# Performance work log

Measured on AMD Instinct MI355X. Metric: run time of the kernel, lower is better.

The kernel has to match this reference:

```python
import jax, jax.numpy as jnp
import numpy as np

D = 1024      # in_features
H = 8         # heads per branch (head_num // 2)
DH = (D // 2) // H  # 64
OUT = 1024

def _split_heads(x, B, S):
    # [B, S, D/2] -> [B, H, S, DH]
    return x.reshape(B, S, H, DH).transpose(0, 2, 1, 3)

def _attn(q, k, v):
    # q,k,v: [B, H, S, DH]
    scores = jnp.einsum('bhqd,bhkd->bhqk', q, k) / jnp.sqrt(jnp.float32(DH))
    a = jax.nn.softmax(scores, axis=-1)
    return jnp.einsum('bhqk,bhkd->bhqd', a, v)

def setup_inputs() -> dict:
    key = jax.random.key(0)
    ks = jax.random.split(key, 16)
    B, S = 2, 2048
    d2 = D // 2
    sc = lambda fan_in: 1.0 / np.sqrt(fan_in)
    inp = {
        'f1': jax.random.normal(ks[0], (B, S, D), jnp.float32),
        'f2': jax.random.normal(ks[1], (B, S, D), jnp.float32),
    }
    names = ['qs', 'ks', 'vs', 'qc', 'kc', 'vc']
    for i, n in enumerate(names):
        inp['W' + n] = jax.random.uniform(ks[2 + i], (d2, D), jnp.float32, -sc(D), sc(D))
        inp['b' + n] = jax.random.uniform(ks[8 + i], (d2,), jnp.float32, -sc(D), sc(D))
    inp['Wo'] = jax.random.uniform(ks[14], (OUT, 2 * D), jnp.float32, -sc(2 * D), sc(2 * D))
    inp['bo'] = jax.random.uniform(ks[15], (OUT,), jnp.float32, -sc(2 * D), sc(2 * D))
    return inp

def reference(f1, f2, Wqs, bqs, Wks, bks, Wvs, bvs, Wqc, bqc, Wkc, bkc, Wvc, bvc, Wo, bo):
    B, S, _ = f1.shape
    lin = lambda x, W, b: jax.nn.relu(x @ W.T + b)
    qs = lin(f1, Wqs, bqs); ks_ = lin(f1, Wks, bks); vs = lin(f1, Wvs, bvs)
    qc = lin(f1, Wqc, bqc); kc = lin(f2, Wkc, bkc); vc = lin(f2, Wvc, bvc)
    ys = _attn(_split_heads(qs, B, S), _split_heads(ks_, B, S), _split_heads(vs, B, S))
    yc = _attn(_split_heads(qc, B, S), _split_heads(kc, B, S), _split_heads(vc, B, S))
    merge = lambda y: y.transpose(0, 2, 1, 3).reshape(B, S, D // 2)
    # reshape_to_batches followed by reshape_from_batches on vs/vc is identity
    y = jnp.concatenate([merge(ys), merge(yc), vs, vc], axis=-1)  # [B, S, 2D]
    return jax.nn.relu(y @ Wo.T + bo)
```

## Files before the change

kernel.cpp:

```cpp
#include <hip/hip_runtime.h>
#include <hip/hip_bf16.h>

using bf16 = __hip_bfloat16;
typedef __attribute__((ext_vector_type(8))) short bf16x8;
typedef __attribute__((ext_vector_type(4))) float f32x4;
typedef __attribute__((ext_vector_type(16))) float f32x16;
typedef __attribute__((ext_vector_type(4))) unsigned int u32x4;

#define MTOT 4096

__device__ __forceinline__ f32x4 fzero() {
    f32x4 z = {0.f, 0.f, 0.f, 0.f};
    return z;
}
__device__ __forceinline__ f32x16 fzero16() {
    f32x16 z = {0.f,0.f,0.f,0.f,0.f,0.f,0.f,0.f,0.f,0.f,0.f,0.f,0.f,0.f,0.f,0.f};
    return z;
}

__device__ __forceinline__ f32x4 mfma16(bf16x8 a, bf16x8 b, f32x4 c) {
    return __builtin_amdgcn_mfma_f32_16x16x32_bf16(a, b, c, 0, 0, 0);
}
__device__ __forceinline__ f32x16 mfma32(bf16x8 a, bf16x8 b, f32x16 c) {
    return __builtin_amdgcn_mfma_f32_32x32x16_bf16(a, b, c, 0, 0, 0);
}

__device__ __forceinline__ float exp2_raw(float x) {
    float r;
    asm("v_exp_f32 %0, %1" : "=v"(r) : "v"(x));
    return r;
}

typedef const __attribute__((address_space(1))) unsigned int* gas_ptr;
typedef __attribute__((address_space(3))) unsigned int* las_ptr;
__device__ __forceinline__ void async_copy16(const bf16* g, bf16* l) {
    __builtin_amdgcn_global_load_lds((gas_ptr)(const void*)g, (las_ptr)(void*)l, 16, 0, 0);
}

__device__ __forceinline__ bf16x8 load8(const bf16* p) {
    return *(const bf16x8*)p;
}
__device__ __forceinline__ bf16x8 load8(const float* p) {
    float4 a = *(const float4*)p;
    float4 b = *(const float4*)(p + 4);
    bf16 t[8];
    t[0] = __float2bfloat16(a.x); t[1] = __float2bfloat16(a.y);
    t[2] = __float2bfloat16(a.z); t[3] = __float2bfloat16(a.w);
    t[4] = __float2bfloat16(b.x); t[5] = __float2bfloat16(b.y);
    t[6] = __float2bfloat16(b.z); t[7] = __float2bfloat16(b.w);
    return *(const bf16x8*)t;
}

__device__ __forceinline__ void store_out(bf16* C, size_t idx, float v) {
    C[idx] = __float2bfloat16(v);
}
__device__ __forceinline__ void store_out(float* C, size_t idx, float v) {
    C[idx] = v;
}

__global__ void MultiHeadSelfCrossAttention_7834020348638_kernel(float* out, int n) {
    int i = blockIdx.x * blockDim.x + threadIdx.x;
    if (i < n) out[i] = 0.25f;
}

struct CvtArgs {
    const float* src[9];
    bf16* dst[9];
    int n8[9];
};
__global__ void cvt_kernel(CvtArgs a) {
    int seg = blockIdx.y;
    int t = blockIdx.x * blockDim.x + threadIdx.x;
    if (t < a.n8[seg])
        *(bf16x8*)(a.dst[seg] + (size_t)t * 8) = load8(a.src[seg] + (size_t)t * 8);
}

template <int BN, typename TC>
__device__ __forceinline__ void gemm_fast(
    const bf16* __restrict__ A, int lda,
    const bf16* __restrict__ Bt, int ldb,
    const float* __restrict__ bias,
    TC* __restrict__ C, int ldc,
    int K, int m0, int n0)
{
    constexpr int NI  = BN / 32;
    constexpr int ACH = 128 * 64 / 8 / 256;
    constexpr int BCH = BN * 64 / 8 / 256;

    __shared__ bf16 As[128 * 64];
    __shared__ bf16 Bs[BN * 64];

    const int tid  = threadIdx.x;
    const int lane = tid & 63;
    const int l15  = lane & 15, quad = lane >> 4;
    const int wave = tid >> 6;
    const int wr   = wave >> 1, wc = wave & 1;

    f32x4 acc[4][NI];
#pragma unroll
    for (int mi = 0; mi < 4; mi++)
#pragma unroll
        for (int ni = 0; ni < NI; ni++)
            acc[mi][ni] = fzero();

    for (int k0 = 0; k0 < K; k0 += 64) {
        __syncthreads();
#pragma unroll
        for (int i = 0; i < ACH; i++) {
            int idx = i * 256 + tid;
            int r   = idx >> 3;
            int cg  = (idx & 7) * 8;
            async_copy16(A + (size_t)(m0 + r) * lda + k0 + cg, &As[idx * 8]);
        }
#pragma unroll
        for (int i = 0; i < BCH; i++) {
            int idx = i * 256 + tid;
            int r   = idx >> 3;
            int cg  = (idx & 7) * 8;
            async_copy16(Bt + (size_t)(n0 + r) * ldb + k0 + cg, &Bs[idx * 8]);
        }
        __syncthreads();

#pragma unroll
        for (int ks = 0; ks < 2; ks++) {
            bf16x8 af[4], bfr[NI];
#pragma unroll
            for (int mi = 0; mi < 4; mi++)
                af[mi] = *(const bf16x8*)&As[(wr * 64 + mi * 16 + l15) * 64 + ks * 32 + quad * 8];
#pragma unroll
            for (int ni = 0; ni < NI; ni++)
                bfr[ni] = *(const bf16x8*)&Bs[(wc * (BN / 2) + ni * 16 + l15) * 64 + ks * 32 + quad * 8];
#pragma unroll
            for (int mi = 0; mi < 4; mi++)
#pragma unroll
                for (int ni = 0; ni < NI; ni++)
                    acc[mi][ni] = mfma16(af[mi], bfr[ni], acc[mi][ni]);
        }
    }

#pragma unroll
    for (int ni = 0; ni < NI; ni++) {
        int col = n0 + wc * (BN / 2) + ni * 16 + l15;
        float bb = bias[col];
#pragma unroll
        for (int mi = 0; mi < 4; mi++) {
#pragma unroll
            for (int r = 0; r < 4; r++) {
                int row = m0 + wr * 64 + mi * 16 + quad * 4 + r;
                store_out(C, (size_t)row * ldc + col, fmaxf(acc[mi][ni][r] + bb, 0.f));
            }
        }
    }
}

template <int BN, typename TA, typename TB, typename TC>
__device__ __forceinline__ void gemm_reg(
    const TA* __restrict__ A, int lda,
    const TB* __restrict__ Bt, int ldb,
    const float* __restrict__ bias,
    TC* __restrict__ C, int ldc,
    int K, int m0, int n0)
{
    constexpr int NI  = BN / 32;
    constexpr int BCH = BN * 4 / 256;

    __shared__ bf16 As[128 * 32];
    __shared__ bf16 Bs[BN * 32];

    const int tid  = threadIdx.x;
    const int lane = tid & 63;
    const int l15  = lane & 15, quad = lane >> 4;
    const int wave = tid >> 6;
    const int wr   = wave >> 1, wc = wave & 1;

    f32x4 acc[4][NI];
#pragma unroll
    for (int mi = 0; mi < 4; mi++)
#pragma unroll
        for (int ni = 0; ni < NI; ni++)
            acc[mi][ni] = fzero();

    for (int k0 = 0; k0 < K; k0 += 32) {
        bf16x8 ra[2], rb[BCH];
#pragma unroll
        for (int i = 0; i < 2; i++) {
            int idx = i * 256 + tid;
            ra[i] = load8(A + (size_t)(m0 + (idx >> 2)) * lda + k0 + (idx & 3) * 8);
        }
#pragma unroll
        for (int i = 0; i < BCH; i++) {
            int idx = i * 256 + tid;
            rb[i] = load8(Bt + (size_t)(n0 + (idx >> 2)) * ldb + k0 + (idx & 3) * 8);
        }
        __syncthreads();
#pragma unroll
        for (int i = 0; i < 2; i++)
            *(bf16x8*)&As[(i * 256 + tid) * 8] = ra[i];
#pragma unroll
        for (int i = 0; i < BCH; i++)
            *(bf16x8*)&Bs[(i * 256 + tid) * 8] = rb[i];
        __syncthreads();

        bf16x8 af[4], bfr[NI];
#pragma unroll
        for (int mi = 0; mi < 4; mi++)
            af[mi] = *(const bf16x8*)&As[(wr * 64 + mi * 16 + l15) * 32 + quad * 8];
#pragma unroll
        for (int ni = 0; ni < NI; ni++)
            bfr[ni] = *(const bf16x8*)&Bs[(wc * (BN / 2) + ni * 16 + l15) * 32 + quad * 8];
#pragma unroll
        for (int mi = 0; mi < 4; mi++)
#pragma unroll
            for (int ni = 0; ni < NI; ni++)
                acc[mi][ni] = mfma16(af[mi], bfr[ni], acc[mi][ni]);
    }

#pragma unroll
    for (int ni = 0; ni < NI; ni++) {
        int col = n0 + wc * (BN / 2) + ni * 16 + l15;
        float bb = bias[col];
#pragma unroll
        for (int mi = 0; mi < 4; mi++) {
#pragma unroll
            for (int r = 0; r < 4; r++) {
                int row = m0 + wr * 64 + mi * 16 + quad * 4 + r;
                store_out(C, (size_t)row * ldc + col, fmaxf(acc[mi][ni][r] + bb, 0.f));
            }
        }
    }
}

__global__ void proj_fast(
    const bf16* __restrict__ F1, const bf16* __restrict__ F2,
    const bf16* __restrict__ Wb,
    const float* __restrict__ bqs, const float* __restrict__ bks,
    const float* __restrict__ bvs, const float* __restrict__ bqc,
    const float* __restrict__ bkc, const float* __restrict__ bvc,
    bf16* __restrict__ Y, bf16* Qs, bf16* Ks, bf16* Qc, bf16* Kc)
{
    const int g = blockIdx.z;
    const bf16* X; const float* bi; bf16* C; int ldc;
    switch (g) {
        case 0:  X = F1; bi = bqs; C = Qs;       ldc = 512;  break;
        case 1:  X = F1; bi = bks; C = Ks;       ldc = 512;  break;
        case 2:  X = F1; bi = bvs; C = Y + 1024; ldc = 2048; break;
        case 3:  X = F1; bi = bqc; C = Qc;       ldc = 512;  break;
        case 4:  X = F2; bi = bkc; C = Kc;       ldc = 512;  break;
        default: X = F2; bi = bvc; C = Y + 1536; ldc = 2048; break;
    }
    gemm_fast<128, bf16>(X, 1024, Wb + (size_t)g * 512 * 1024, 1024, bi, C, ldc,
                         1024, blockIdx.y * 128, blockIdx.x * 128);
}

__global__ void out_fast(const bf16* __restrict__ Y, const bf16* __restrict__ WoB,
                         const float* __restrict__ bo, float* __restrict__ out)
{
    gemm_fast<64, float>(Y, 2048, WoB, 2048, bo, out, 1024, 2048,
                         blockIdx.y * 128, blockIdx.x * 64);
}

__global__ void proj_reg(
    const float* __restrict__ f1, const float* __restrict__ f2,
    const float* __restrict__ Wqs, const float* __restrict__ bqs,
    const float* __restrict__ Wks, const float* __restrict__ bks,
    const float* __restrict__ Wvs, const float* __restrict__ bvs,
    const float* __restrict__ Wqc, const float* __restrict__ bqc,
    const float* __restrict__ Wkc, const float* __restrict__ bkc,
    const float* __restrict__ Wvc, const float* __restrict__ bvc,
    bf16* __restrict__ Y, bf16* Qs, bf16* Ks, bf16* Qc, bf16* Kc)
{
    const int g = blockIdx.z;
    const float *X, *W, *bi; bf16* C; int ldc;
    switch (g) {
        case 0:  X = f1; W = Wqs; bi = bqs; C = Qs;       ldc = 512;  break;
        case 1:  X = f1; W = Wks; bi = bks; C = Ks;       ldc = 512;  break;
        case 2:  X = f1; W = Wvs; bi = bvs; C = Y + 1024; ldc = 2048; break;
        case 3:  X = f1; W = Wqc; bi = bqc; C = Qc;       ldc = 512;  break;
        case 4:  X = f2; W = Wkc; bi = bkc; C = Kc;       ldc = 512;  break;
        default: X = f2; W = Wvc; bi = bvc; C = Y + 1536; ldc = 2048; break;
    }
    gemm_reg<128>(X, 1024, W, 1024, bi, C, ldc, 1024, blockIdx.y * 128, blockIdx.x * 128);
}

__global__ void out_reg(const bf16* __restrict__ Y, const float* __restrict__ Wo,
                        const float* __restrict__ bo, float* __restrict__ out)
{
    gemm_reg<64>(Y, 2048, Wo, 2048, bo, out, 1024, 2048, blockIdx.y * 128, blockIdx.x * 64);
}

__global__ void vt_kernel(const bf16* __restrict__ Y, bf16* __restrict__ VT) {
    const int tid = threadIdx.x;
    const int st = blockIdx.x, bh = blockIdx.y, br = blockIdx.z;
    const int b = bh >> 3, h = bh & 7;
    const bf16* src = Y + (size_t)b * 2048 * 2048 + 1024 + br * 512 + h * 64;
    bf16* dst = VT + ((size_t)((br * 2 + b) * 8 + h)) * 64 * 2048;
    const int s0 = st * 64;
#pragma unroll
    for (int i = 0; i < 2; i++) {
        int idx = i * 256 + tid;
        int d = idx >> 3, cs = (idx & 7) * 8;
        bf16 tmp[8];
#pragma unroll
        for (int j = 0; j < 8; j++)
            tmp[j] = src[(size_t)(s0 + cs + j) * 2048 + d];
        *(bf16x8*)&dst[(size_t)d * 2048 + s0 + cs] = *(const bf16x8*)tmp;
    }
}

__global__ __launch_bounds__(256, 4) void attn2_kernel(
    const bf16* __restrict__ Qsb, const bf16* __restrict__ Ksb,
    const bf16* __restrict__ Qcb, const bf16* __restrict__ Kcb,
    const bf16* __restrict__ VT, bf16* __restrict__ Y)
{
    __shared__ bf16 SMEM[4][64 * 64];

    const int tid  = threadIdx.x;
    const int lane = tid & 63;
    const int l31  = lane & 31;
    const int hi   = lane >> 5;
    const int wave = tid >> 6;

    const int lid   = blockIdx.x + 16 * blockIdx.y + 256 * blockIdx.z;
    const int xcd   = lid & 7, slot = lid >> 3;
    const int combo = xcd + 8 * (slot >> 4);
    const int qt    = slot & 15;
    const int bh    = combo & 15, br = combo >> 4;
    const int b = bh >> 3, h = bh & 7;

    const bf16* Qb = (br ? Qcb : Qsb) + (size_t)b * 2048 * 512 + h * 64;
    const bf16* Kb = (br ? Kcb : Ksb) + (size_t)b * 2048 * 512 + h * 64;
    const bf16* Vt = VT + ((size_t)((br * 2 + b) * 8 + h)) * 64 * 2048;
    bf16*       Ob = Y + (size_t)b * 2048 * 2048 + br * 512 + h * 64;
    const int q0 = qt * 128;

    bf16* QP = &SMEM[0][0];

#pragma unroll
    for (int i = 0; i < 4; i++) {
        int idx = i * 256 + tid;
        int r = idx >> 3, c0 = (idx & 7) * 8;
        *(bf16x8*)&QP[r * 72 + c0] = *(const bf16x8*)&Qb[(size_t)(q0 + r) * 512 + c0];
    }
    __syncthreads();

    bf16x8 qf[4];
#pragma unroll
    for (int kq = 0; kq < 4; kq++)
        qf[kq] = *(const bf16x8*)&QP[(wave * 32 + l31) * 72 + kq * 16 + hi * 8];
    __syncthreads();

#pragma unroll
    for (int i = 0; i < 2; i++) {
        int idx = i * 256 + tid;
        int r = idx >> 3, sl = (idx & 7) ^ (r & 7);
        async_copy16(Kb + (size_t)r * 512 + sl * 8, &SMEM[0][idx * 8]);
    }
#pragma unroll
    for (int i = 0; i < 2; i++) {
        int idx = i * 256 + tid;
        int r = idx >> 3, sl = (idx & 7) ^ (r & 7);
        async_copy16(Vt + (size_t)r * 2048 + sl * 8, &SMEM[1][idx * 8]);
    }
    __syncthreads();

    const short one_bits = (l31 == 0) ? (short)0x3F80 : (short)0;
    bf16x8 onesA;
#pragma unroll
    for (int j = 0; j < 8; j++) onesA[j] = one_bits;

    f32x16 o[2], ol;
    o[0] = fzero16(); o[1] = fzero16(); ol = fzero16();

    const float C1 = 0.18033688011112043f;
    const float C2 = -5.7707801635558535f;

    for (int jt = 0; jt < 32; jt++) {
        const int cur = jt & 1;
        const bf16* Kc = &SMEM[cur * 2][0];
        const bf16* Vc = &SMEM[cur * 2 + 1][0];

        if (jt < 31) {
            const size_t s0n = (size_t)(jt + 1) * 64;
            bf16* Kn = &SMEM[(cur ^ 1) * 2][0];
            bf16* Vn = &SMEM[(cur ^ 1) * 2 + 1][0];
#pragma unroll
            for (int i = 0; i < 2; i++) {
                int idx = i * 256 + tid;
                int r = idx >> 3, sl = (idx & 7) ^ (r & 7);
                async_copy16(Kb + (s0n + r) * 512 + sl * 8, &Kn[idx * 8]);
            }
#pragma unroll
            for (int i = 0; i < 2; i++) {
                int idx = i * 256 + tid;
                int r = idx >> 3, sl = (idx & 7) ^ (r & 7);
                async_copy16(Vt + (size_t)r * 2048 + s0n + sl * 8, &Vn[idx * 8]);
            }
        }

        f32x16 st[2];
        st[0] = fzero16(); st[1] = fzero16();
        __builtin_amdgcn_s_setprio(1);
#pragma unroll
        for (int t = 0; t < 2; t++)
#pragma unroll
            for (int kq = 0; kq < 4; kq++) {
                bf16x8 kf = *(const bf16x8*)&Kc[(t * 32 + l31) * 64
                               + (((kq * 2 + hi) ^ (l31 & 7)) * 8)];
                st[t] = mfma32(kf, qf[kq], st[t]);
            }
        __builtin_amdgcn_s_setprio(0);

        unsigned int pk[2][4][2];
#pragma unroll
        for (int t = 0; t < 2; t++)
#pragma unroll
            for (int g = 0; g < 4; g++) {
                float e0 = exp2_raw(fmaf(st[t][4 * g + 0], C1, C2));
                float e1 = exp2_raw(fmaf(st[t][4 * g + 1], C1, C2));
                float e2 = exp2_raw(fmaf(st[t][4 * g + 2], C1, C2));
                float e3 = exp2_raw(fmaf(st[t][4 * g + 3], C1, C2));
                asm("v_cvt_pk_bf16_f32 %0, %1, %2"
                    : "=v"(pk[t][g][0]) : "v"(e0), "v"(e1));
                asm("v_cvt_pk_bf16_f32 %0, %1, %2"
                    : "=v"(pk[t][g][1]) : "v"(e2), "v"(e3));
            }

        __builtin_amdgcn_s_setprio(1);
#pragma unroll
        for (int kb = 0; kb < 4; kb++) {
            const int t = kb >> 1, gb = (kb & 1) * 2;
            unsigned int u0 = pk[t][gb][0],     u1 = pk[t][gb][1];
            unsigned int v0 = pk[t][gb + 1][0], v1 = pk[t][gb + 1][1];
            asm("v_permlane32_swap_b32 %0, %1" : "+v"(u0), "+v"(v0));
            asm("v_permlane32_swap_b32 %0, %1" : "+v"(u1), "+v"(v1));
            u32x4 pw; pw.x = u0; pw.y = u1; pw.z = v0; pw.w = v1;
            bf16x8 pfrag = __builtin_bit_cast(bf16x8, pw);
#pragma unroll
            for (int dt = 0; dt < 2; dt++) {
                bf16x8 vf = *(const bf16x8*)&Vc[(dt * 32 + l31) * 64
                               + (((kb * 2 + hi) ^ (l31 & 7)) * 8)];
                o[dt] = mfma32(vf, pfrag, o[dt]);
            }
            ol = mfma32(onesA, pfrag, ol);
        }
        __builtin_amdgcn_s_setprio(0);

        __syncthreads();
    }

    const float linv = 1.0f / __shfl(ol[0], l31);
#pragma unroll
    for (int dt = 0; dt < 2; dt++)
#pragma unroll
        for (int r = 0; r < 16; r++) {
            int d = dt * 32 + (r & 3) + 8 * (r >> 2) + 4 * hi;
            QP[(wave * 32 + l31) * 72 + d] = __float2bfloat16(o[dt][r] * linv);
        }
    __syncthreads();
#pragma unroll
    for (int i = 0; i < 4; i++) {
        int idx = i * 256 + tid;
        int r = idx >> 3, c0 = (idx & 7) * 8;
        *(bf16x8*)&Ob[(size_t)(q0 + r) * 2048 + c0] = *(const bf16x8*)&QP[r * 72 + c0];
    }
}

__global__ __launch_bounds__(256, 4) void attn_kernel(
    const bf16* __restrict__ Qsb, const bf16* __restrict__ Ksb,
    const bf16* __restrict__ Qcb, const bf16* __restrict__ Kcb,
    bf16* __restrict__ Y)
{
    __shared__ bf16 QP[64 * 72];
    __shared__ bf16 Ksh[64 * 72];
    __shared__ bf16 Vsh[64 * 72];

    const int tid  = threadIdx.x;
    const int lane = tid & 63;
    const int l15  = lane & 15, quad = lane >> 4;
    const int wave = tid >> 6;
    const int qt = blockIdx.x, bh = blockIdx.y, br = blockIdx.z;
    const int b = bh >> 3, h = bh & 7;

    const bf16* Qb = (br ? Qcb : Qsb) + (size_t)b * 2048 * 512 + h * 64;
    const bf16* Kb = (br ? Kcb : Ksb) + (size_t)b * 2048 * 512 + h * 64;
    const bf16* Vb = Y + (size_t)b * 2048 * 2048 + 1024 + br * 512 + h * 64;
    bf16*       Ob = Y + (size_t)b * 2048 * 2048 +        br * 512 + h * 64;
    const int q0 = qt * 64;

#pragma unroll
    for (int i = 0; i < 2; i++) {
        int idx = i * 256 + tid;
        int r = idx >> 3, c0 = (idx & 7) * 8;
        *(bf16x8*)&QP[r * 72 + c0] = *(const bf16x8*)&Qb[(size_t)(q0 + r) * 512 + c0];
    }
    __syncthreads();

    bf16x8 qf[2];
#pragma unroll
    for (int ks = 0; ks < 2; ks++)
        qf[ks] = *(const bf16x8*)&QP[(wave * 16 + l15) * 72 + ks * 32 + quad * 8];

    const short one_bits = l15 == 0 ? (short)0x3F80 : (short)0;
    bf16x8 onesf;
#pragma unroll
    for (int j = 0; j < 8; j++) onesf[j] = one_bits;

    f32x4 o[4], o_l;
    o_l = fzero();
#pragma unroll
    for (int ni = 0; ni < 4; ni++) o[ni] = fzero();

    const int kr0 = tid >> 3, kc0 = (tid & 7) * 8;
    const int kr1 = (256 + tid) >> 3;

    bf16x8 kr[2], vr[2];
    kr[0] = *(const bf16x8*)&Kb[(size_t)kr0 * 512 + kc0];
    kr[1] = *(const bf16x8*)&Kb[(size_t)kr1 * 512 + kc0];
    vr[0] = *(const bf16x8*)&Vb[(size_t)lane * 2048 + (0 * 4 + wave) * 8];
    vr[1] = *(const bf16x8*)&Vb[(size_t)lane * 2048 + (1 * 4 + wave) * 8];

    for (int jt = 0; jt < 32; jt++) {
        __syncthreads();
        *(bf16x8*)&Ksh[kr0 * 72 + kc0] = kr[0];
        *(bf16x8*)&Ksh[kr1 * 72 + kc0] = kr[1];
#pragma unroll
        for (int i = 0; i < 2; i++) {
            int cg = i * 4 + wave;
            const bf16* e = (const bf16*)&vr[i];
#pragma unroll
            for (int j = 0; j < 8; j++)
                Vsh[(cg * 8 + j) * 72 + lane] = e[j];
        }
        __syncthreads();

        {
            const int s0n = (jt < 31) ? (jt + 1) * 64 : 31 * 64;
            kr[0] = *(const bf16x8*)&Kb[(size_t)(s0n + kr0) * 512 + kc0];
            kr[1] = *(const bf16x8*)&Kb[(size_t)(s0n + kr1) * 512 + kc0];
            vr[0] = *(const bf16x8*)&Vb[(size_t)(s0n + lane) * 2048 + (0 * 4 + wave) * 8];
            vr[1] = *(const bf16x8*)&Vb[(size_t)(s0n + lane) * 2048 + (1 * 4 + wave) * 8];
        }

        f32x4 s[4];
#pragma unroll
        for (int ni = 0; ni < 4; ni++) s[ni] = fzero();
#pragma unroll
        for (int ni = 0; ni < 4; ni++)
#pragma unroll
            for (int ks = 0; ks < 2; ks++) {
                bf16x8 kf = *(const bf16x8*)&Ksh[(ni * 16 + l15) * 72 + ks * 32 + quad * 8];
                s[ni] = mfma16(qf[ks], kf, s[ni]);
            }

#pragma unroll
        for (int ni = 0; ni < 4; ni++)
#pragma unroll
            for (int r = 0; r < 4; r++) {
                float p = __expf(s[ni][r] * 0.125f - 4.0f);
                QP[(wave * 16 + quad * 4 + r) * 72 + ni * 16 + l15] = __float2bfloat16(p);
            }

#pragma unroll
        for (int ks = 0; ks < 2; ks++) {
            bf16x8 pf = *(const bf16x8*)&QP[(wave * 16 + l15) * 72 + ks * 32 + quad * 8];
#pragma unroll
            for (int ni = 0; ni < 4; ni++) {
                bf16x8 vf = *(const bf16x8*)&Vsh[(ni * 16 + l15) * 72 + ks * 32 + quad * 8];
                o[ni] = mfma16(pf, vf, o[ni]);
            }
            o_l = mfma16(pf, onesf, o_l);
        }
    }

#pragma unroll
    for (int r = 0; r < 4; r++) {
        float lsum = __shfl(o_l[r], quad << 4);
        float inv = 1.f / lsum;
        int row = q0 + wave * 16 + quad * 4 + r;
#pragma unroll
        for (int ni = 0; ni < 4; ni++)
            Ob[(size_t)row * 2048 + ni * 16 + l15] = __float2bfloat16(o[ni][r] * inv);
    }
}

extern "C" void kernel_launch(void* const* d_in, const int* in_sizes, int n_in,
                              void* d_out, int out_size, void* d_ws, size_t ws_size,
                              hipStream_t stream) {
    const size_t out_bytes = (size_t)out_size * sizeof(float);
    const size_t ws_base = ((size_t)MTOT * 2048 + 4 * (size_t)MTOT * 512) * 2;
    const size_t ws_fast = ws_base + ((size_t)2 * MTOT * 1024 + 6 * 512 * 1024 + 1024 * 2048) * 2;
    const size_t vt_elems = (size_t)2 * 2 * 8 * 64 * 2048;
    const size_t ws_fast2 = ws_fast + vt_elems * 2;

    if (n_in != 16) { hipMemsetAsync(d_out, 0x43, out_bytes, stream); return; }
    if (ws_size < ws_base) { hipMemsetAsync(d_out, 0x41, out_bytes, stream); return; }

    const float* f1  = (const float*)d_in[0];
    const float* f2  = (const float*)d_in[1];
    const float* Wqs = (const float*)d_in[2];  const float* bqs = (const float*)d_in[3];
    const float* Wks = (const float*)d_in[4];  const float* bks = (const float*)d_in[5];
    const float* Wvs = (const float*)d_in[6];  const float* bvs = (const float*)d_in[7];
    const float* Wqc = (const float*)d_in[8];  const float* bqc = (const float*)d_in[9];
    const float* Wkc = (const float*)d_in[10]; const float* bkc = (const float*)d_in[11];
    const float* Wvc = (const float*)d_in[12]; const float* bvc = (const float*)d_in[13];
    const float* Wo  = (const float*)d_in[14]; const float* bo  = (const float*)d_in[15];

    bf16* Y  = (bf16*)d_ws;
    bf16* Qs = Y  + (size_t)MTOT * 2048;
    bf16* Ks = Qs + (size_t)MTOT * 512;
    bf16* Qc = Ks + (size_t)MTOT * 512;
    bf16* Kc = Qc + (size_t)MTOT * 512;
    float* out = (float*)d_out;

    if (ws_size >= ws_fast) {
        bf16* F1  = Kc + (size_t)MTOT * 512;
        bf16* F2  = F1 + (size_t)MTOT * 1024;
        bf16* Wb  = F2 + (size_t)MTOT * 1024;
        bf16* WoB = Wb + (size_t)6 * 512 * 1024;
        bf16* VT  = WoB + (size_t)1024 * 2048;

        CvtArgs ca;
        ca.src[0] = f1;  ca.dst[0] = F1;  ca.n8[0] = MTOT * 1024 / 8;
        ca.src[1] = f2;  ca.dst[1] = F2;  ca.n8[1] = MTOT * 1024 / 8;
        const float* ws_[6] = {Wqs, Wks, Wvs, Wqc, Wkc, Wvc};
        for (int i = 0; i < 6; i++) {
            ca.src[2 + i] = ws_[i];
            ca.dst[2 + i] = Wb + (size_t)i * 512 * 1024;
            ca.n8[2 + i]  = 512 * 1024 / 8;
        }
        ca.src[8] = Wo; ca.dst[8] = WoB; ca.n8[8] = 1024 * 2048 / 8;

        cvt_kernel<<<dim3((MTOT * 1024 / 8 + 255) / 256, 9), 256, 0, stream>>>(ca);
        proj_fast<<<dim3(4, 32, 6), 256, 0, stream>>>(
            F1, F2, Wb, bqs, bks, bvs, bqc, bkc, bvc, Y, Qs, Ks, Qc, Kc);
        if (ws_size >= ws_fast2) {
            vt_kernel<<<dim3(32, 16, 2), 256, 0, stream>>>(Y, VT);
            attn2_kernel<<<dim3(16, 16, 2), 256, 0, stream>>>(Qs, Ks, Qc, Kc, VT, Y);
        } else {
            attn_kernel<<<dim3(32, 16, 2), 256, 0, stream>>>(Qs, Ks, Qc, Kc, Y);
        }
        out_fast<<<dim3(16, 32), 256, 0, stream>>>(Y, WoB, bo, out);
    } else {
        proj_reg<<<dim3(4, 32, 6), 256, 0, stream>>>(
            f1, f2, Wqs, bqs, Wks, bks, Wvs, bvs, Wqc, bqc, Wkc, bkc, Wvc, bvc,
            Y, Qs, Ks, Qc, Kc);
        attn_kernel<<<dim3(32, 16, 2), 256, 0, stream>>>(Qs, Ks, Qc, Kc, Y);
        out_reg<<<dim3(16, 32), 256, 0, stream>>>(Y, Wo, bo, out);
    }
}
```

Measured before the change: 233.3 us.

## Fuse V transpose into projection epilogue and shrink GEMM tiles for occupancy

Removes the separate vt_kernel by having the projection GEMM epilogue write the transposed V (per head, d-major) directly into the VT buffer alongside the normal row-major output. The projection tile shrinks from 128x128 to 128x64 and the output GEMM tile from 128x64 to 64x64, with launch_bounds(256,4) on both, to launch more blocks and raise occupancy. This trades a kernel launch and an extra read of Y for scattered 8-byte transposed stores and smaller tiles with less data reuse per block.

```diff
diff --git a/kernel.cpp b/kernel.cpp
--- a/kernel.cpp
+++ b/kernel.cpp
@@ -3,6 +3,7 @@
 
 using bf16 = __hip_bfloat16;
 typedef __attribute__((ext_vector_type(8))) short bf16x8;
+typedef __attribute__((ext_vector_type(4))) short s16x4;
 typedef __attribute__((ext_vector_type(4))) float f32x4;
 typedef __attribute__((ext_vector_type(16))) float f32x16;
 typedef __attribute__((ext_vector_type(4))) unsigned int u32x4;
@@ -56,6 +57,9 @@
 }
 __device__ __forceinline__ void store_out(float* C, size_t idx, float v) {
     C[idx] = v;
+}
+__device__ __forceinline__ short bf16_bits(float v) {
+    return __builtin_bit_cast(short, __float2bfloat16(v));
 }
 
 __global__ void MultiHeadSelfCrossAttention_7834020348638_kernel(float* out, int n) {
@@ -75,19 +79,20 @@
         *(bf16x8*)(a.dst[seg] + (size_t)t * 8) = load8(a.src[seg] + (size_t)t * 8);
 }
 
-template <int BN, typename TC>
+template <int BM, int BN, typename TC>
 __device__ __forceinline__ void gemm_fast(
     const bf16* __restrict__ A, int lda,
     const bf16* __restrict__ Bt, int ldb,
     const float* __restrict__ bias,
     TC* __restrict__ C, int ldc,
-    int K, int m0, int n0)
-{
+    int K, int m0, int n0, bf16* __restrict__ VTW)
+{
+    constexpr int MI  = BM / 32;
     constexpr int NI  = BN / 32;
-    constexpr int ACH = 128 * 64 / 8 / 256;
+    constexpr int ACH = BM * 64 / 8 / 256;
     constexpr int BCH = BN * 64 / 8 / 256;
 
-    __shared__ bf16 As[128 * 64];
+    __shared__ bf16 As[BM * 64];
     __shared__ bf16 Bs[BN * 64];
 
     const int tid  = threadIdx.x;
@@ -96,9 +101,9 @@
     const int wave = tid >> 6;
     const int wr   = wave >> 1, wc = wave & 1;
 
-    f32x4 acc[4][NI];
-#pragma unroll
-    for (int mi = 0; mi < 4; mi++)
+    f32x4 acc[MI][NI];
+#pragma unroll
+    for (int mi = 0; mi < MI; mi++)
 #pragma unroll
         for (int ni = 0; ni < NI; ni++)
             acc[mi][ni] = fzero();
@@ -123,15 +128,15 @@
 
 #pragma unroll
         for (int ks = 0; ks < 2; ks++) {
-            bf16x8 af[4], bfr[NI];
-#pragma unroll
-            for (int mi = 0; mi < 4; mi++)
-                af[mi] = *(const bf16x8*)&As[(wr * 64 + mi * 16 + l15) * 64 + ks * 32 + quad * 8];
+            bf16x8 af[MI], bfr[NI];
+#pragma unroll
+            for (int mi = 0; mi < MI; mi++)
+                af[mi] = *(const bf16x8*)&As[(wr * (BM / 2) + mi * 16 + l15) * 64 + ks * 32 + quad * 8];
 #pragma unroll
             for (int ni = 0; ni < NI; ni++)
                 bfr[ni] = *(const bf16x8*)&Bs[(wc * (BN / 2) + ni * 16 + l15) * 64 + ks * 32 + quad * 8];
 #pragma unroll
-            for (int mi = 0; mi < 4; mi++)
+            for (int mi = 0; mi < MI; mi++)
 #pragma unroll
                 for (int ni = 0; ni < NI; ni++)
                     acc[mi][ni] = mfma16(af[mi], bfr[ni], acc[mi][ni]);
@@ -143,11 +148,21 @@
         int col = n0 + wc * (BN / 2) + ni * 16 + l15;
         float bb = bias[col];
 #pragma unroll
-        for (int mi = 0; mi < 4; mi++) {
-#pragma unroll
-            for (int r = 0; r < 4; r++) {
-                int row = m0 + wr * 64 + mi * 16 + quad * 4 + r;
-                store_out(C, (size_t)row * ldc + col, fmaxf(acc[mi][ni][r] + bb, 0.f));
+        for (int mi = 0; mi < MI; mi++) {
+            float v0 = fmaxf(acc[mi][ni][0] + bb, 0.f);
+            float v1 = fmaxf(acc[mi][ni][1] + bb, 0.f);
+            float v2 = fmaxf(acc[mi][ni][2] + bb, 0.f);
+            float v3 = fmaxf(acc[mi][ni][3] + bb, 0.f);
+            int row0 = m0 + wr * (BM / 2) + mi * 16 + quad * 4;
+            store_out(C, (size_t)(row0 + 0) * ldc + col, v0);
+            store_out(C, (size_t)(row0 + 1) * ldc + col, v1);
+            store_out(C, (size_t)(row0 + 2) * ldc + col, v2);
+            store_out(C, (size_t)(row0 + 3) * ldc + col, v3);
+            if (VTW) {
+                int d = wc * (BN / 2) + ni * 16 + l15;
+                int s = row0 & 2047;
+                short tv[4] = {bf16_bits(v0), bf16_bits(v1), bf16_bits(v2), bf16_bits(v3)};
+                *(s16x4*)&VTW[(size_t)d * 2048 + s] = *(const s16x4*)tv;
             }
         }
     }
@@ -230,13 +245,14 @@
     }
 }
 
-__global__ void proj_fast(
+__global__ __launch_bounds__(256, 4) void proj_fast(
     const bf16* __restrict__ F1, const bf16* __restrict__ F2,
     const bf16* __restrict__ Wb,
     const float* __restrict__ bqs, const float* __restrict__ bks,
     const float* __restrict__ bvs, const float* __restrict__ bqc,
     const float* __restrict__ bkc, const float* __restrict__ bvc,
-    bf16* __restrict__ Y, bf16* Qs, bf16* Ks, bf16* Qc, bf16* Kc)
+    bf16* __restrict__ Y, bf16* Qs, bf16* Ks, bf16* Qc, bf16* Kc,
+    bf16* __restrict__ VT)
 {
     const int g = blockIdx.z;
     const bf16* X; const float* bi; bf16* C; int ldc;
@@ -248,15 +264,24 @@
         case 4:  X = F2; bi = bkc; C = Kc;       ldc = 512;  break;
         default: X = F2; bi = bvc; C = Y + 1536; ldc = 2048; break;
     }
-    gemm_fast<128, bf16>(X, 1024, Wb + (size_t)g * 512 * 1024, 1024, bi, C, ldc,
-                         1024, blockIdx.y * 128, blockIdx.x * 128);
-}
-
-__global__ void out_fast(const bf16* __restrict__ Y, const bf16* __restrict__ WoB,
-                         const float* __restrict__ bo, float* __restrict__ out)
-{
-    gemm_fast<64, float>(Y, 2048, WoB, 2048, bo, out, 1024, 2048,
-                         blockIdx.y * 128, blockIdx.x * 64);
+    const int m0 = blockIdx.y * 128, n0 = blockIdx.x * 64;
+    bf16* vtw = nullptr;
+    if (VT && (g == 2 || g == 5)) {
+        const int br = (g == 5);
+        const int b  = m0 >> 11;
+        const int h  = n0 >> 6;
+        vtw = VT + ((size_t)((br * 2 + b) * 8 + h)) * 64 * 2048;
+    }
+    gemm_fast<128, 64, bf16>(X, 1024, Wb + (size_t)g * 512 * 1024, 1024, bi, C, ldc,
+                             1024, m0, n0, vtw);
+}
+
+__global__ __launch_bounds__(256, 4) void out_fast(
+    const bf16* __restrict__ Y, const bf16* __restrict__ WoB,
+    const float* __restrict__ bo, float* __restrict__ out)
+{
+    gemm_fast<64, 64, float>(Y, 2048, WoB, 2048, bo, out, 1024, 2048,
+                             blockIdx.y * 64, blockIdx.x * 64, nullptr);
 }
 
 __global__ void proj_reg(
@@ -288,25 +313,6 @@
     gemm_reg<64>(Y, 2048, Wo, 2048, bo, out, 1024, 2048, blockIdx.y * 128, blockIdx.x * 64);
 }
 
-__global__ void vt_kernel(const bf16* __restrict__ Y, bf16* __restrict__ VT) {
-    const int tid = threadIdx.x;
-    const int st = blockIdx.x, bh = blockIdx.y, br = blockIdx.z;
-    const int b = bh >> 3, h = bh & 7;
-    const bf16* src = Y + (size_t)b * 2048 * 2048 + 1024 + br * 512 + h * 64;
-    bf16* dst = VT + ((size_t)((br * 2 + b) * 8 + h)) * 64 * 2048;
-    const int s0 = st * 64;
-#pragma unroll
-    for (int i = 0; i < 2; i++) {
-        int idx = i * 256 + tid;
-        int d = idx >> 3, cs = (idx & 7) * 8;
-        bf16 tmp[8];
-#pragma unroll
-        for (int j = 0; j < 8; j++)
-            tmp[j] = src[(size_t)(s0 + cs + j) * 2048 + d];
-        *(bf16x8*)&dst[(size_t)d * 2048 + s0 + cs] = *(const bf16x8*)tmp;
-    }
-}
-
 __global__ __launch_bounds__(256, 4) void attn2_kernel(
     const bf16* __restrict__ Qsb, const bf16* __restrict__ Ksb,
     const bf16* __restrict__ Qcb, const bf16* __restrict__ Kcb,
@@ -618,6 +624,7 @@
         bf16* Wb  = F2 + (size_t)MTOT * 1024;
         bf16* WoB = Wb + (size_t)6 * 512 * 1024;
         bf16* VT  = WoB + (size_t)1024 * 2048;
+        const bool fast2 = (ws_size >= ws_fast2);
 
         CvtArgs ca;
         ca.src[0] = f1;  ca.dst[0] = F1;  ca.n8[0] = MTOT * 1024 / 8;
@@ -631,15 +638,15 @@
         ca.src[8] = Wo; ca.dst[8] = WoB; ca.n8[8] = 1024 * 2048 / 8;
 
         cvt_kernel<<<dim3((MTOT * 1024 / 8 + 255) / 256, 9), 256, 0, stream>>>(ca);
-        proj_fast<<<dim3(4, 32, 6), 256, 0, stream>>>(
-            F1, F2, Wb, bqs, bks, bvs, bqc, bkc, bvc, Y, Qs, Ks, Qc, Kc);
-        if (ws_size >= ws_fast2) {
-            vt_kernel<<<dim3(32, 16, 2), 256, 0, stream>>>(Y, VT);
+        proj_fast<<<dim3(8, 32, 6), 256, 0, stream>>>(
+            F1, F2, Wb, bqs, bks, bvs, bqc, bkc, bvc, Y, Qs, Ks, Qc, Kc,
+            fast2 ? VT : nullptr);
+        if (fast2) {
             attn2_kernel<<<dim3(16, 16, 2), 256, 0, stream>>>(Qs, Ks, Qc, Kc, VT, Y);
         } else {
             attn_kernel<<<dim3(32, 16, 2), 256, 0, stream>>>(Qs, Ks, Qc, Kc, Y);
         }
-        out_fast<<<dim3(16, 32), 256, 0, stream>>>(Y, WoB, bo, out);
+        out_fast<<<dim3(16, 64), 256, 0, stream>>>(Y, WoB, bo, out);
     } else {
         proj_reg<<<dim3(4, 32, 6), 256, 0, stream>>>(
             f1, f2, Wqs, bqs, Wks, bks, Wvs, bvs, Wqc, bqc, Wkc, bkc, Wvc, bvc,
```

Result: slower. 245.7 us (+5.3%).
